# Performance work log

Hardware: AMD Instinct MI355X
Metric: run time of the kernel (lower is better)

The kernel has to match this reference:

```python
import jax, jax.numpy as jnp
import numpy as np

N = 100000      # nodes
E = 3200000     # edges
IN_DIM = 128
HID = 128
OUT_DIM = 1
LAYERS = 8
ALPHA = 0.1
THETA = 0.5


def setup_inputs() -> dict:
    key = jax.random.key(0)
    ks = jax.random.split(key, 8)
    x = jax.random.normal(ks[0], (N, IN_DIM), dtype=jnp.float32)
    edge_index = jax.random.randint(ks[1], (2, E), 0, N, dtype=jnp.int64)
    edge_weight = jax.random.uniform(ks[2], (E,), dtype=jnp.float32)  # unused by original forward path
    W_in = jax.random.normal(ks[3], (IN_DIM, HID), dtype=jnp.float32) * 0.05
    b_in = jnp.zeros((HID,), dtype=jnp.float32)
    W_gcn = jax.random.normal(ks[4], (LAYERS, HID, HID), dtype=jnp.float32) * 0.05
    W_out = jax.random.normal(ks[5], (HID, OUT_DIM), dtype=jnp.float32) * 0.05
    b_out = jnp.zeros((OUT_DIM,), dtype=jnp.float32)
    return {"x": x, "edge_weight": edge_weight, "W_in": W_in, "b_in": b_in,
            "W_gcn": W_gcn, "W_out": W_out, "b_out": b_out, "edge_index": edge_index}


def _gcn_norm(edge_index, dtype):
    # add self loops (fill value 1), symmetric normalization deg^-1/2 A deg^-1/2
    sl = jnp.arange(N, dtype=edge_index.dtype)
    row = jnp.concatenate([edge_index[0], sl])
    col = jnp.concatenate([edge_index[1], sl])
    w = jnp.ones(row.shape[0], dtype=dtype)
    deg = jax.ops.segment_sum(w, col, num_segments=N)
    dinv = jnp.where(deg > 0, jax.lax.rsqrt(deg), 0.0)
    norm = dinv[row] * dinv[col]
    return row, col, norm


def reference(x, edge_weight, W_in, b_in, W_gcn, W_out, b_out, edge_index):
    row, col, norm = _gcn_norm(edge_index, x.dtype)
    h = x @ W_in + b_in            # initial_proj
    h0 = h                          # residual x0
    for i in range(LAYERS):
        # dropout is identity in eval mode
        msg = h[row] * norm[:, None]                       # gather + scale [E+N, HID]
        agg = jax.ops.segment_sum(msg, col, num_segments=N)
        s = (1.0 - ALPHA) * agg + ALPHA * h0               # identity-mapped residual
        beta = float(np.log(THETA / (i + 1) + 1.0))
        h = (1.0 - beta) * s + beta * (s @ W_gcn[i])       # GCNII weight mix
        h = jax.nn.relu(h)
    return h @ W_out + b_out
```

## Files before the change

### kernel.cpp

```cpp
#include <hip/hip_runtime.h>
#include <hip/hip_bf16.h>
#include <math.h>

#define N_NODES 100000
#define N_EDGES 3200000
#define HID 128
#define LAYERS 8
#define ALPHA 0.1f
#define THETA 0.5f

#define SCAN_TILE 1024
#define NB_SCAN ((N_NODES + SCAN_TILE - 1) / SCAN_TILE)

typedef unsigned int uint;
typedef unsigned short ushort;
typedef __attribute__((ext_vector_type(8))) short short8;
typedef __attribute__((ext_vector_type(4))) float f32x4;

__device__ inline float bf_lo(uint p) { return __uint_as_float(p << 16); }
__device__ inline float bf_hi(uint p) { return __uint_as_float(p & 0xffff0000u); }
__device__ inline uint bf_pack(float x, float y) {
    uint ux = __float_as_uint(x), uy = __float_as_uint(y);
    uint rx = (ux + 0x7fffu + ((ux >> 16) & 1u)) >> 16;
    uint ry = (uy + 0x7fffu + ((uy >> 16) & 1u)) >> 16;
    return rx | (ry << 16);
}
__device__ inline ushort bfr(float x) {
    uint u = __float_as_uint(x);
    return (ushort)((u + 0x7fffu + ((u >> 16) & 1u)) >> 16);
}
__device__ inline float bff(ushort s) { return __uint_as_float(((uint)s) << 16); }

__global__ __launch_bounds__(256) void k_count(const int* __restrict__ col,
                                               int* __restrict__ cnt) {
    int e = blockIdx.x * 256 + threadIdx.x;
    if (e < N_EDGES) atomicAdd(&cnt[col[e]], 1);
}

__global__ __launch_bounds__(256) void k_dinv(const int* __restrict__ cnt,
                                              float* __restrict__ dinv) {
    int n = blockIdx.x * 256 + threadIdx.x;
    if (n < N_NODES) dinv[n] = rsqrtf((float)(cnt[n] + 1));
}

__global__ __launch_bounds__(256) void k_scan1(const int* __restrict__ cnt,
                                               int* __restrict__ indptr,
                                               int* __restrict__ bsum) {
    __shared__ int lds[256];
    int t = threadIdx.x;
    int base = blockIdx.x * SCAN_TILE + t * 4;
    int v[4];
    int s = 0;
#pragma unroll
    for (int j = 0; j < 4; ++j) {
        v[j] = (base + j < N_NODES) ? cnt[base + j] : 0;
        s += v[j];
    }
    lds[t] = s;
    __syncthreads();
    for (int off = 1; off < 256; off <<= 1) {
        int u = (t >= off) ? lds[t - off] : 0;
        __syncthreads();
        lds[t] += u;
        __syncthreads();
    }
    int excl = lds[t] - s;
    int run = excl;
#pragma unroll
    for (int j = 0; j < 4; ++j) {
        if (base + j < N_NODES) indptr[base + j] = run;
        run += v[j];
    }
    if (t == 255) bsum[blockIdx.x] = lds[255];
}

__global__ __launch_bounds__(256) void k_scan2(const int* __restrict__ bsum,
                                               int* __restrict__ boff) {
    __shared__ int lds[256];
    int t = threadIdx.x;
    int v = (t < NB_SCAN) ? bsum[t] : 0;
    lds[t] = v;
    __syncthreads();
    for (int off = 1; off < 256; off <<= 1) {
        int u = (t >= off) ? lds[t - off] : 0;
        __syncthreads();
        lds[t] += u;
        __syncthreads();
    }
    boff[t] = lds[t] - v;
}

__global__ __launch_bounds__(256) void k_scan3(int* __restrict__ indptr,
                                               const int* __restrict__ boff) {
    int base = blockIdx.x * SCAN_TILE + threadIdx.x * 4;
    int add = boff[blockIdx.x];
#pragma unroll
    for (int j = 0; j < 4; ++j) {
        if (base + j < N_NODES) indptr[base + j] += add;
    }
    if (blockIdx.x == 0 && threadIdx.x == 0) indptr[N_NODES] = N_EDGES;
}

__global__ __launch_bounds__(256) void k_fill(const int* __restrict__ rowi,
                                              const int* __restrict__ coli,
                                              const float* __restrict__ dinv,
                                              const int* __restrict__ indptr,
                                              int* __restrict__ cursor,
                                              int2* __restrict__ csr) {
    int e = blockIdx.x * 256 + threadIdx.x;
    if (e >= N_EDGES) return;
    int r = rowi[e];
    int c = coli[e];
    int p = indptr[c] + atomicAdd(&cursor[c], 1);
    csr[p] = make_int2(r, __float_as_int(dinv[r] * dinv[c]));
}

__global__ __launch_bounds__(256) void k_wprep(const float* __restrict__ Wg,
                                               ushort* __restrict__ Wt) {
    int l = blockIdx.x;
    const float* W = Wg + (size_t)l * HID * HID;
    ushort* T = Wt + (size_t)l * HID * HID;
    int t = threadIdx.x;
#pragma unroll
    for (int i = 0; i < 16; ++i) {
        int idx = t + 256 * i;
        int k = idx >> 5;
        int c4 = idx & 31;
        float4 v = *(const float4*)(W + (size_t)k * HID + c4 * 4);
        T[(c4 * 4 + 0) * HID + k] = bfr(v.x);
        T[(c4 * 4 + 1) * HID + k] = bfr(v.y);
        T[(c4 * 4 + 2) * HID + k] = bfr(v.z);
        T[(c4 * 4 + 3) * HID + k] = bfr(v.w);
    }
}

__global__ __launch_bounds__(256) void k_spmm(const uint* __restrict__ h,
                                              const uint* __restrict__ h0,
                                              const float* __restrict__ dinv,
                                              const int* __restrict__ indptr,
                                              const int2* __restrict__ csr,
                                              uint* __restrict__ s_out) {
    int node = blockIdx.x * 4 + (threadIdx.x >> 6);
    if (node >= N_NODES) return;
    int lane = threadIdx.x & 63;
    int beg = indptr[node];
    int end = indptr[node + 1];
    float ax[8], ay[8];
#pragma unroll
    for (int j = 0; j < 8; ++j) { ax[j] = 0.f; ay[j] = 0.f; }
    int e = beg;
    for (; e + 8 <= end; e += 8) {
        int2 rr[8];
#pragma unroll
        for (int j = 0; j < 8; ++j) rr[j] = csr[e + j];
        uint p[8];
#pragma unroll
        for (int j = 0; j < 8; ++j) p[j] = h[rr[j].x * 64 + lane];
#pragma unroll
        for (int j = 0; j < 8; ++j) {
            float w = __int_as_float(rr[j].y);
            ax[j] = fmaf(w, bf_lo(p[j]), ax[j]);
            ay[j] = fmaf(w, bf_hi(p[j]), ay[j]);
        }
    }
    for (; e < end; ++e) {
        int2 r = csr[e];
        uint pp = h[r.x * 64 + lane];
        float w = __int_as_float(r.y);
        ax[0] = fmaf(w, bf_lo(pp), ax[0]);
        ay[0] = fmaf(w, bf_hi(pp), ay[0]);
    }
    float sum0 = ((ax[0] + ax[1]) + (ax[2] + ax[3])) + ((ax[4] + ax[5]) + (ax[6] + ax[7]));
    float sum1 = ((ay[0] + ay[1]) + (ay[2] + ay[3])) + ((ay[4] + ay[5]) + (ay[6] + ay[7]));
    float di = dinv[node];
    float selfw = di * di;
    uint hs = h[node * 64 + lane];
    uint h0v = h0[node * 64 + lane];
    float rx = (1.0f - ALPHA) * fmaf(selfw, bf_lo(hs), sum0) + ALPHA * bf_lo(h0v);
    float ry = (1.0f - ALPHA) * fmaf(selfw, bf_hi(hs), sum1) + ALPHA * bf_hi(h0v);
    s_out[node * 64 + lane] = bf_pack(rx, ry);
}

__global__ __launch_bounds__(256) void k_gemm_in(const float* __restrict__ A,
                                                 const float* __restrict__ W,
                                                 const float* __restrict__ bias,
                                                 uint* __restrict__ out0,
                                                 uint* __restrict__ out1) {
    __shared__ float sT[32 * 64];
    __shared__ float Ws[32 * 128];
    int t = threadIdx.x;
    int tr = t & 15;
    int tc = t >> 4;
    int rowBase = blockIdx.x * 64;
    float acc[4][8] = {};

    for (int ko = 0; ko < HID; ko += 32) {
#pragma unroll
        for (int pass = 0; pass < 2; ++pass) {
            int lin = t + 256 * pass;
            int r = lin >> 3;
            int kq = lin & 7;
            int ar = rowBase + r;
            if (ar >= N_NODES) ar = N_NODES - 1;
            float4 v = *(const float4*)(A + (size_t)ar * HID + ko + 4 * kq);
            sT[(4 * kq + 0) * 64 + r] = v.x;
            sT[(4 * kq + 1) * 64 + r] = v.y;
            sT[(4 * kq + 2) * 64 + r] = v.z;
            sT[(4 * kq + 3) * 64 + r] = v.w;
        }
#pragma unroll
        for (int pass = 0; pass < 4; ++pass) {
            int lin = t + 256 * pass;
            int k = lin >> 5;
            int c4 = lin & 31;
            *(float4*)&Ws[k * 128 + 4 * c4] =
                *(const float4*)(W + (size_t)(ko + k) * HID + 4 * c4);
        }
        __syncthreads();
#pragma unroll
        for (int k = 0; k < 32; ++k) {
            float4 a = *(const float4*)&sT[k * 64 + 4 * tr];
            float4 w0 = *(const float4*)&Ws[k * 128 + 8 * tc];
            float4 w1 = *(const float4*)&Ws[k * 128 + 8 * tc + 4];
            float av[4] = {a.x, a.y, a.z, a.w};
            float wv[8] = {w0.x, w0.y, w0.z, w0.w, w1.x, w1.y, w1.z, w1.w};
#pragma unroll
            for (int i = 0; i < 4; ++i)
#pragma unroll
                for (int j = 0; j < 8; ++j)
                    acc[i][j] = fmaf(av[i], wv[j], acc[i][j]);
        }
        __syncthreads();
    }

    int c0 = 8 * tc;
    float bb[8];
#pragma unroll
    for (int j = 0; j < 8; ++j) bb[j] = bias[c0 + j];
#pragma unroll
    for (int i = 0; i < 4; ++i) {
        int r = rowBase + 4 * tr + i;
        if (r >= N_NODES) break;
        float v[8];
#pragma unroll
        for (int j = 0; j < 8; ++j) v[j] = acc[i][j] + bb[j];
        uint4 o;
        o.x = bf_pack(v[0], v[1]);
        o.y = bf_pack(v[2], v[3]);
        o.z = bf_pack(v[4], v[5]);
        o.w = bf_pack(v[6], v[7]);
        *(uint4*)(out0 + (size_t)r * 64 + c0 / 2) = o;
        *(uint4*)(out1 + (size_t)r * 64 + c0 / 2) = o;
    }
}

#define SAS 136

__global__ __launch_bounds__(256) void k_gemm_layer(const uint* __restrict__ A,
                                                    const ushort* __restrict__ Wt,
                                                    uint* __restrict__ out0,
                                                    float beta) {
    __shared__ ushort sA[64 * SAS];
    __shared__ ushort sW[128 * SAS];
    int t = threadIdx.x;
    int lane = t & 63;
    int wv = t >> 6;
    int rowBase = blockIdx.x * 64;

#pragma unroll
    for (int i = 0; i < 4; ++i) {
        int idx = t + 256 * i;
        int r = idx >> 4;
        int q = idx & 15;
        int ar = rowBase + r;
        if (ar >= N_NODES) ar = N_NODES - 1;
        uint4 v = *(const uint4*)(A + (size_t)ar * 64 + q * 4);
        *(uint4*)((uint*)(sA + r * SAS) + q * 4) = v;
    }
#pragma unroll
    for (int i = 0; i < 8; ++i) {
        int idx = t + 256 * i;
        int r = idx >> 4;
        int q = idx & 15;
        uint4 v = *(const uint4*)((const uint*)(Wt + (size_t)r * HID) + q * 4);
        *(uint4*)((uint*)(sW + r * SAS) + q * 4) = v;
    }
    __syncthreads();

    int fr = lane & 15;
    int fq = lane >> 4;
    f32x4 acc[4][2] = {};
#pragma unroll
    for (int kc = 0; kc < 4; ++kc) {
        int kof = kc * 32 + fq * 8;
        short8 b0 = *(const short8*)(sW + (wv * 32 + fr) * SAS + kof);
        short8 b1 = *(const short8*)(sW + (wv * 32 + 16 + fr) * SAS + kof);
#pragma unroll
        for (int tm = 0; tm < 4; ++tm) {
            short8 a = *(const short8*)(sA + (tm * 16 + fr) * SAS + kof);
            acc[tm][0] = __builtin_amdgcn_mfma_f32_16x16x32_bf16(a, b0, acc[tm][0], 0, 0, 0);
            acc[tm][1] = __builtin_amdgcn_mfma_f32_16x16x32_bf16(a, b1, acc[tm][1], 0, 0, 0);
        }
    }
    __syncthreads();

    ushort* pack = sW;
    float ob = 1.0f - beta;
#pragma unroll
    for (int tm = 0; tm < 4; ++tm)
#pragma unroll
        for (int tn = 0; tn < 2; ++tn)
#pragma unroll
            for (int r = 0; r < 4; ++r) {
                int row = tm * 16 + fq * 4 + r;
                int col = wv * 32 + tn * 16 + fr;
                float sv = bff(sA[row * SAS + col]);
                float val = fmaxf(fmaf(ob, sv, beta * acc[tm][tn][r]), 0.f);
                pack[row * 128 + col] = bfr(val);
            }
    __syncthreads();
#pragma unroll
    for (int i = 0; i < 4; ++i) {
        int idx = t + 256 * i;
        int r = idx >> 4;
        int q = idx & 15;
        int ar = rowBase + r;
        if (ar < N_NODES)
            *(uint4*)(out0 + (size_t)ar * 64 + q * 4) =
                *(const uint4*)((const uint*)(pack + r * 128) + q * 4);
    }
}

__global__ __launch_bounds__(256) void k_out(const uint* __restrict__ h,
                                             const float* __restrict__ W_out,
                                             const float* __restrict__ b_out,
                                             float* __restrict__ out) {
    int node = blockIdx.x * 4 + (threadIdx.x >> 6);
    if (node >= N_NODES) return;
    int lane = threadIdx.x & 63;
    uint p = h[node * 64 + lane];
    float2 wv = *(const float2*)(W_out + lane * 2);
    float pr = bf_lo(p) * wv.x + bf_hi(p) * wv.y;
#pragma unroll
    for (int off = 32; off > 0; off >>= 1) pr += __shfl_down(pr, off);
    if (lane == 0) out[node] = pr + b_out[0];
}

extern "C" void kernel_launch(void* const* d_in, const int* in_sizes, int n_in,
                              void* d_out, int out_size, void* d_ws, size_t ws_size,
                              hipStream_t stream) {
    const float* x     = (const float*)d_in[0];
    const float* W_in  = (const float*)d_in[2];
    const float* b_in  = (const float*)d_in[3];
    const float* W_gcn = (const float*)d_in[4];
    const float* W_out = (const float*)d_in[5];
    const float* b_out = (const float*)d_in[6];
    const int*   ei    = (const int*)d_in[7];
    const int* rowi = ei;
    const int* coli = ei + N_EDGES;
    float* out = (float*)d_out;

    char* ws = (char*)d_ws;
    auto alloc = [&](size_t bytes) -> char* {
        char* p = ws;
        ws += (bytes + 255) & ~(size_t)255;
        return p;
    };
    int*    cnt     = (int*)   alloc((size_t)N_NODES * 4);
    float*  dinv    = (float*) alloc((size_t)N_NODES * 4);
    int*    indptr  = (int*)   alloc((size_t)(N_NODES + 1) * 4);
    int*    cursor  = (int*)   alloc((size_t)N_NODES * 4);
    int*    bsum    = (int*)   alloc(1024 * 4);
    int*    boff    = (int*)   alloc(1024 * 4);
    int2*   csr     = (int2*)  alloc((size_t)N_EDGES * 8);
    ushort* Wt      = (ushort*)alloc((size_t)LAYERS * HID * HID * 2);
    uint*   hA      = (uint*)  alloc((size_t)N_NODES * 64 * 4);
    uint*   hB      = (uint*)  alloc((size_t)N_NODES * 64 * 4);
    uint*   h0      = (uint*)  alloc((size_t)N_NODES * 64 * 4);

    hipMemsetAsync(cnt, 0, (size_t)N_NODES * 4, stream);
    hipMemsetAsync(cursor, 0, (size_t)N_NODES * 4, stream);

    k_count<<<(N_EDGES + 255) / 256, 256, 0, stream>>>(coli, cnt);
    k_dinv<<<(N_NODES + 255) / 256, 256, 0, stream>>>(cnt, dinv);
    k_scan1<<<NB_SCAN, 256, 0, stream>>>(cnt, indptr, bsum);
    k_scan2<<<1, 256, 0, stream>>>(bsum, boff);
    k_scan3<<<NB_SCAN, 256, 0, stream>>>(indptr, boff);
    k_fill<<<(N_EDGES + 255) / 256, 256, 0, stream>>>(rowi, coli, dinv, indptr,
                                                      cursor, csr);
    k_wprep<<<LAYERS, 256, 0, stream>>>(W_gcn, Wt);

    int gemm_blocks = (N_NODES + 63) / 64;
    k_gemm_in<<<gemm_blocks, 256, 0, stream>>>(x, W_in, b_in, h0, hA);

    for (int l = 0; l < LAYERS; ++l) {
        k_spmm<<<(N_NODES + 3) / 4, 256, 0, stream>>>(hA, h0, dinv, indptr,
                                                      csr, hB);
        float beta = logf(THETA / (float)(l + 1) + 1.0f);
        k_gemm_layer<<<gemm_blocks, 256, 0, stream>>>(
            hB, Wt + (size_t)l * HID * HID, hA, beta);
    }
    k_out<<<(N_NODES + 3) / 4, 256, 0, stream>>>(hA, W_out, b_out, out);
}
```

Before: 1.559 ms.

## Shard CSR build atomics 8 ways and deepen SpMM gather unroll

Degree counting and CSR fill now spread atomics over 8 per-node shard slots chosen by block index, with the prefix scan run over the expanded shard array, to reduce atomic contention on popular destinations. The SpMM loop gathers 16 neighbours per iteration instead of 8 and handles the remainder in padded groups of 4 with zero weights, raising memory-level parallelism. It costs an 8x larger count/indptr array and scan, plus more registers in SpMM.

```diff
diff --git a/kernel.cpp b/kernel.cpp
--- a/kernel.cpp
+++ b/kernel.cpp
@@ -9,8 +9,10 @@
 #define ALPHA 0.1f
 #define THETA 0.5f
 
-#define SCAN_TILE 1024
-#define NB_SCAN ((N_NODES + SCAN_TILE - 1) / SCAN_TILE)
+#define SH 8
+#define NODES8 (N_NODES * SH)
+#define SCAN_TILE 4096
+#define NB_SCAN ((NODES8 + SCAN_TILE - 1) / SCAN_TILE)
 
 typedef unsigned int uint;
 typedef unsigned short ushort;
@@ -32,28 +34,33 @@
 __device__ inline float bff(ushort s) { return __uint_as_float(((uint)s) << 16); }
 
 __global__ __launch_bounds__(256) void k_count(const int* __restrict__ col,
-                                               int* __restrict__ cnt) {
+                                               int* __restrict__ cnt8) {
     int e = blockIdx.x * 256 + threadIdx.x;
-    if (e < N_EDGES) atomicAdd(&cnt[col[e]], 1);
-}
-
-__global__ __launch_bounds__(256) void k_dinv(const int* __restrict__ cnt,
+    int shard = blockIdx.x & (SH - 1);
+    if (e < N_EDGES) atomicAdd(&cnt8[col[e] * SH + shard], 1);
+}
+
+__global__ __launch_bounds__(256) void k_dinv(const int* __restrict__ cnt8,
                                               float* __restrict__ dinv) {
     int n = blockIdx.x * 256 + threadIdx.x;
-    if (n < N_NODES) dinv[n] = rsqrtf((float)(cnt[n] + 1));
-}
-
-__global__ __launch_bounds__(256) void k_scan1(const int* __restrict__ cnt,
-                                               int* __restrict__ indptr,
+    if (n >= N_NODES) return;
+    int4 a = *(const int4*)(cnt8 + n * SH);
+    int4 b = *(const int4*)(cnt8 + n * SH + 4);
+    int deg = a.x + a.y + a.z + a.w + b.x + b.y + b.z + b.w;
+    dinv[n] = rsqrtf((float)(deg + 1));
+}
+
+__global__ __launch_bounds__(256) void k_scan1(const int* __restrict__ cnt8,
+                                               int* __restrict__ indptr8,
                                                int* __restrict__ bsum) {
     __shared__ int lds[256];
     int t = threadIdx.x;
-    int base = blockIdx.x * SCAN_TILE + t * 4;
-    int v[4];
+    int base = blockIdx.x * SCAN_TILE + t * 16;
+    int v[16];
     int s = 0;
 #pragma unroll
-    for (int j = 0; j < 4; ++j) {
-        v[j] = (base + j < N_NODES) ? cnt[base + j] : 0;
+    for (int j = 0; j < 16; ++j) {
+        v[j] = (base + j < NODES8) ? cnt8[base + j] : 0;
         s += v[j];
     }
     lds[t] = s;
@@ -64,11 +71,10 @@
         lds[t] += u;
         __syncthreads();
     }
-    int excl = lds[t] - s;
-    int run = excl;
-#pragma unroll
-    for (int j = 0; j < 4; ++j) {
-        if (base + j < N_NODES) indptr[base + j] = run;
+    int run = lds[t] - s;
+#pragma unroll
+    for (int j = 0; j < 16; ++j) {
+        if (base + j < NODES8) indptr8[base + j] = run;
         run += v[j];
     }
     if (t == 255) bsum[blockIdx.x] = lds[255];
@@ -90,28 +96,30 @@
     boff[t] = lds[t] - v;
 }
 
-__global__ __launch_bounds__(256) void k_scan3(int* __restrict__ indptr,
+__global__ __launch_bounds__(256) void k_scan3(int* __restrict__ indptr8,
                                                const int* __restrict__ boff) {
-    int base = blockIdx.x * SCAN_TILE + threadIdx.x * 4;
+    int base = blockIdx.x * SCAN_TILE + threadIdx.x * 16;
     int add = boff[blockIdx.x];
 #pragma unroll
-    for (int j = 0; j < 4; ++j) {
-        if (base + j < N_NODES) indptr[base + j] += add;
-    }
-    if (blockIdx.x == 0 && threadIdx.x == 0) indptr[N_NODES] = N_EDGES;
+    for (int j = 0; j < 16; ++j) {
+        if (base + j < NODES8) indptr8[base + j] += add;
+    }
+    if (blockIdx.x == 0 && threadIdx.x == 0) indptr8[NODES8] = N_EDGES;
 }
 
 __global__ __launch_bounds__(256) void k_fill(const int* __restrict__ rowi,
                                               const int* __restrict__ coli,
                                               const float* __restrict__ dinv,
-                                              const int* __restrict__ indptr,
-                                              int* __restrict__ cursor,
+                                              const int* __restrict__ indptr8,
+                                              int* __restrict__ cursor8,
                                               int2* __restrict__ csr) {
     int e = blockIdx.x * 256 + threadIdx.x;
     if (e >= N_EDGES) return;
+    int shard = blockIdx.x & (SH - 1);
     int r = rowi[e];
     int c = coli[e];
-    int p = indptr[c] + atomicAdd(&cursor[c], 1);
+    int slot = c * SH + shard;
+    int p = indptr8[slot] + atomicAdd(&cursor8[slot], 1);
     csr[p] = make_int2(r, __float_as_int(dinv[r] * dinv[c]));
 }
 
@@ -137,45 +145,56 @@
 __global__ __launch_bounds__(256) void k_spmm(const uint* __restrict__ h,
                                               const uint* __restrict__ h0,
                                               const float* __restrict__ dinv,
-                                              const int* __restrict__ indptr,
+                                              const int* __restrict__ indptr8,
                                               const int2* __restrict__ csr,
                                               uint* __restrict__ s_out) {
     int node = blockIdx.x * 4 + (threadIdx.x >> 6);
     if (node >= N_NODES) return;
     int lane = threadIdx.x & 63;
-    int beg = indptr[node];
-    int end = indptr[node + 1];
+    int beg = indptr8[node * SH];
+    int end = indptr8[node * SH + SH];
+    float di = dinv[node];
+    uint hs = h[node * 64 + lane];
+    uint h0v = h0[node * 64 + lane];
     float ax[8], ay[8];
 #pragma unroll
     for (int j = 0; j < 8; ++j) { ax[j] = 0.f; ay[j] = 0.f; }
     int e = beg;
-    for (; e + 8 <= end; e += 8) {
-        int2 rr[8];
-#pragma unroll
-        for (int j = 0; j < 8; ++j) rr[j] = csr[e + j];
-        uint p[8];
-#pragma unroll
-        for (int j = 0; j < 8; ++j) p[j] = h[rr[j].x * 64 + lane];
-#pragma unroll
-        for (int j = 0; j < 8; ++j) {
+    for (; e + 16 <= end; e += 16) {
+        int2 rr[16];
+#pragma unroll
+        for (int j = 0; j < 16; ++j) rr[j] = csr[e + j];
+        uint p[16];
+#pragma unroll
+        for (int j = 0; j < 16; ++j) p[j] = h[rr[j].x * 64 + lane];
+#pragma unroll
+        for (int j = 0; j < 16; ++j) {
             float w = __int_as_float(rr[j].y);
-            ax[j] = fmaf(w, bf_lo(p[j]), ax[j]);
-            ay[j] = fmaf(w, bf_hi(p[j]), ay[j]);
-        }
-    }
-    for (; e < end; ++e) {
-        int2 r = csr[e];
-        uint pp = h[r.x * 64 + lane];
-        float w = __int_as_float(r.y);
-        ax[0] = fmaf(w, bf_lo(pp), ax[0]);
-        ay[0] = fmaf(w, bf_hi(pp), ay[0]);
+            ax[j & 7] = fmaf(w, bf_lo(p[j]), ax[j & 7]);
+            ay[j & 7] = fmaf(w, bf_hi(p[j]), ay[j & 7]);
+        }
+    }
+    for (; e < end; e += 4) {
+        int2 rr[4];
+        float w[4];
+#pragma unroll
+        for (int j = 0; j < 4; ++j) {
+            int idx = e + j;
+            rr[j] = csr[idx < end ? idx : beg];
+            w[j] = (idx < end) ? __int_as_float(rr[j].y) : 0.f;
+        }
+        uint p[4];
+#pragma unroll
+        for (int j = 0; j < 4; ++j) p[j] = h[rr[j].x * 64 + lane];
+#pragma unroll
+        for (int j = 0; j < 4; ++j) {
+            ax[j] = fmaf(w[j], bf_lo(p[j]), ax[j]);
+            ay[j] = fmaf(w[j], bf_hi(p[j]), ay[j]);
+        }
     }
     float sum0 = ((ax[0] + ax[1]) + (ax[2] + ax[3])) + ((ax[4] + ax[5]) + (ax[6] + ax[7]));
     float sum1 = ((ay[0] + ay[1]) + (ay[2] + ay[3])) + ((ay[4] + ay[5]) + (ay[6] + ay[7]));
-    float di = dinv[node];
     float selfw = di * di;
-    uint hs = h[node * 64 + lane];
-    uint h0v = h0[node * 64 + lane];
     float rx = (1.0f - ALPHA) * fmaf(selfw, bf_lo(hs), sum0) + ALPHA * bf_lo(h0v);
     float ry = (1.0f - ALPHA) * fmaf(selfw, bf_hi(hs), sum1) + ALPHA * bf_hi(h0v);
     s_out[node * 64 + lane] = bf_pack(rx, ry);
@@ -366,10 +385,10 @@
         ws += (bytes + 255) & ~(size_t)255;
         return p;
     };
-    int*    cnt     = (int*)   alloc((size_t)N_NODES * 4);
+    int*    cnt8    = (int*)   alloc((size_t)NODES8 * 4);
     float*  dinv    = (float*) alloc((size_t)N_NODES * 4);
-    int*    indptr  = (int*)   alloc((size_t)(N_NODES + 1) * 4);
-    int*    cursor  = (int*)   alloc((size_t)N_NODES * 4);
+    int*    indptr8 = (int*)   alloc((size_t)(NODES8 + 8) * 4);
+    int*    cursor8 = (int*)   alloc((size_t)NODES8 * 4);
     int*    bsum    = (int*)   alloc(1024 * 4);
     int*    boff    = (int*)   alloc(1024 * 4);
     int2*   csr     = (int2*)  alloc((size_t)N_EDGES * 8);
@@ -378,23 +397,23 @@
     uint*   hB      = (uint*)  alloc((size_t)N_NODES * 64 * 4);
     uint*   h0      = (uint*)  alloc((size_t)N_NODES * 64 * 4);
 
-    hipMemsetAsync(cnt, 0, (size_t)N_NODES * 4, stream);
-    hipMemsetAsync(cursor, 0, (size_t)N_NODES * 4, stream);
-
-    k_count<<<(N_EDGES + 255) / 256, 256, 0, stream>>>(coli, cnt);
-    k_dinv<<<(N_NODES + 255) / 256, 256, 0, stream>>>(cnt, dinv);
-    k_scan1<<<NB_SCAN, 256, 0, stream>>>(cnt, indptr, bsum);
+    hipMemsetAsync(cnt8, 0, (size_t)NODES8 * 4, stream);
+    hipMemsetAsync(cursor8, 0, (size_t)NODES8 * 4, stream);
+
+    k_count<<<(N_EDGES + 255) / 256, 256, 0, stream>>>(coli, cnt8);
+    k_dinv<<<(N_NODES + 255) / 256, 256, 0, stream>>>(cnt8, dinv);
+    k_scan1<<<NB_SCAN, 256, 0, stream>>>(cnt8, indptr8, bsum);
     k_scan2<<<1, 256, 0, stream>>>(bsum, boff);
-    k_scan3<<<NB_SCAN, 256, 0, stream>>>(indptr, boff);
-    k_fill<<<(N_EDGES + 255) / 256, 256, 0, stream>>>(rowi, coli, dinv, indptr,
-                                                      cursor, csr);
+    k_scan3<<<NB_SCAN, 256, 0, stream>>>(indptr8, boff);
+    k_fill<<<(N_EDGES + 255) / 256, 256, 0, stream>>>(rowi, coli, dinv, indptr8,
+                                                      cursor8, csr);
     k_wprep<<<LAYERS, 256, 0, stream>>>(W_gcn, Wt);
 
     int gemm_blocks = (N_NODES + 63) / 64;
     k_gemm_in<<<gemm_blocks, 256, 0, stream>>>(x, W_in, b_in, h0, hA);
 
     for (int l = 0; l < LAYERS; ++l) {
-        k_spmm<<<(N_NODES + 3) / 4, 256, 0, stream>>>(hA, h0, dinv, indptr,
+        k_spmm<<<(N_NODES + 3) / 4, 256, 0, stream>>>(hA, h0, dinv, indptr8,
                                                       csr, hB);
         float beta = logf(THETA / (float)(l + 1) + 1.0f);
         k_gemm_layer<<<gemm_blocks, 256, 0, stream>>>(
```

Result: no change. 1.533 ms (-1.7%).
